# Optimization experiments

Measured on AMD Instinct MI355X. Metric: run time of the kernel, lower is better.

Reference implementation:

```python
import jax, jax.numpy as jnp
import numpy as np
from itertools import combinations

Nt, Nrf, Nk, FEAT, BATCH = 64, 4, 8, 512, 1024
Ng = Nt // Nk                      # 8
_MAX = len(list(combinations(range(Ng), Nrf)))  # 70
CSETSIZE = int(2 ** np.floor(np.log2(_MAX)))    # 64
SQRT_NRF = np.float32(np.sqrt(Nrf))


def _generate_antenna_selection_set(num_target):
    """Max-hamming-distance antenna selection set (numpy, matches torch code)."""
    combs = list(combinations(range(Ng), Nrf))
    maxSize = len(combs)
    globalSet = np.zeros((maxSize, Nt, Nrf), np.float32)
    for i, act in enumerate(combs):
        for j, a in enumerate(act):
            globalSet[i, a * Nk:a * Nk + Nk, j] = 1.0
    gsum = globalSet.sum(-1)  # (maxSize, Nt)
    selectSet = np.zeros((num_target, Nt, Nrf), np.float32)
    available = []
    for idx in range(num_target):
        if len(available) == 0:
            available = list(range(maxSize))
        if idx == 0:
            hd = np.zeros(len(available))
        else:
            sel = selectSet[:idx].sum(-1)            # (idx, Nt)
            cand = gsum[np.array(available)]          # (nAvail, Nt)
            hd = (sel[None, :, :] != cand[:, None, :]).sum(axis=(1, 2))
        sid = available[int(np.argmax(hd))]
        selectSet[idx] = globalSet[sid]
        available.remove(sid)
    return selectSet


def setup_inputs() -> dict:
    key = jax.random.key(0)
    ks = jax.random.split(key, 7)
    s = 1.0 / np.sqrt(FEAT)
    DDIM = CSETSIZE * Nrf * Nrf
    return {
        "x": jax.random.normal(ks[0], (BATCH, FEAT), jnp.float32),
        "W_A": jax.random.normal(ks[1], (Nt, FEAT), jnp.float32) * s,
        "b_A": jax.random.normal(ks[2], (Nt,), jnp.float32) * s,
        "W_Dr": jax.random.normal(ks[3], (DDIM, FEAT), jnp.float32) * s,
        "b_Dr": jax.random.normal(ks[4], (DDIM,), jnp.float32) * s,
        "W_Di": jax.random.normal(ks[5], (DDIM, FEAT), jnp.float32) * s,
        "b_Di": jax.random.normal(ks[6], (DDIM,), jnp.float32) * s,
        "CSet": jnp.asarray(_generate_antenna_selection_set(CSETSIZE)),
    }


def reference(x, W_A, b_A, W_Dr, b_Dr, W_Di, b_Di, CSet):
    B = x.shape[0]
    theta = x @ W_A.T + b_A                          # (B, Nt)
    cosT, sinT = jnp.cos(theta), jnp.sin(theta)
    eye = jnp.eye(Nt, dtype=x.dtype)
    A_real = (cosT[:, :, None] * eye)[:, None]       # (B, 1, Nt, Nt) diag-embed
    A_imag = (sinT[:, :, None] * eye)[:, None]
    D_real = (x @ W_Dr.T + b_Dr).reshape(B, CSETSIZE, Nrf, Nrf)
    D_imag = (x @ W_Di.T + b_Di).reshape(B, CSETSIZE, Nrf, Nrf)
    # diag(cos) @ C == row-scale of C (identical math to the dense matmul)
    ArC = cosT[:, None, :, None] * CSet[None]        # (B, CSetSize, Nt, Nrf)
    AiC = sinT[:, None, :, None] * CSet[None]
    ArCDr = ArC @ D_real
    ArCDi = ArC @ D_imag
    AiCDr = AiC @ D_real
    AiCDi = AiC @ D_imag
    V_real = ArCDr - AiCDi                           # (B, CSetSize, Nt, Nrf)
    V_imag = ArCDi + AiCDr
    V_F = jnp.sqrt(jnp.sum(V_real ** 2 + V_imag ** 2, axis=(2, 3)))
    V_F = V_F[:, :, None, None]
    D_real_n = SQRT_NRF * D_real / V_F
    D_imag_n = SQRT_NRF * D_imag / V_F
    return (A_real, A_imag, D_real_n, D_imag_n, CSet)
```

## Files before the change

### kernel.cpp

```cpp
#include <hip/hip_runtime.h>
#include <math.h>

#define BATCH 1024
#define FEAT  512
#define NT    64
#define DDIM  1024

typedef __attribute__((ext_vector_type(8))) short  short8;
typedef __attribute__((ext_vector_type(4))) short  short4v;
typedef __attribute__((ext_vector_type(4))) float  floatx4;

#define AIMG_OFF  0
#define BIMG_OFF  1048576
#define THETA_OFF 3276800

__device__ __forceinline__ unsigned short bf16rne(float f) {
    unsigned int u = __float_as_uint(f);
    return (unsigned short)((u + 0x7fffu + ((u >> 16) & 1u)) >> 16);
}
__device__ __forceinline__ short4v pack4(const float4 a) {
    short4v r;
    r[0] = (short)bf16rne(a.x); r[1] = (short)bf16rne(a.y);
    r[2] = (short)bf16rne(a.z); r[3] = (short)bf16rne(a.w);
    return r;
}

__device__ __forceinline__ void gld16(const unsigned char* g, unsigned char* l) {
    __builtin_amdgcn_global_load_lds(
        (const __attribute__((address_space(1))) unsigned int*)g,
        (__attribute__((address_space(3))) unsigned int*)l, 16, 0, 0);
}


__global__ __launch_bounds__(256) void k0_prep(
    const float* __restrict__ x,
    const float* __restrict__ W_A,  const float* __restrict__ b_A,
    const float* __restrict__ W_Dr, const float* __restrict__ W_Di,
    const float* __restrict__ cset,
    unsigned char* __restrict__ ws, float* __restrict__ out)
{
    __shared__ __align__(16) unsigned short As[64][40];
    __shared__ __align__(16) unsigned short Bs[64][40];

    const int bid = blockIdx.x;
    const int tid = threadIdx.x;

    if (bid < 256) {
        unsigned short* aimg = (unsigned short*)(ws + AIMG_OFF);
        unsigned short* bimg = (unsigned short*)(ws + BIMG_OFF);
        const int gtid = bid * 256 + tid;
        for (int idx = gtid; idx < 196608; idx += 65536) {
            const float* src;
            unsigned short* dst;
            if (idx < 65536) {
                const int rt = idx >> 12, kb = (idx >> 9) & 7;
                const int r  = (idx >> 3) & 63, c = idx & 7;
                src = x + ((size_t)(rt * 64 + r) * FEAT + kb * 64 + c * 8);
                dst = aimg + ((rt * 8 + kb) * 4096 + r * 64 + ((c ^ (r & 7)) * 8));
            } else {
                const int j  = idx - 65536;
                const int ct = j >> 12, kb = (j >> 9) & 7;
                const int n  = (j >> 3) & 63, c = j & 7;
                const int g = n >> 5, h = (n >> 4) & 1, pos = n & 15;
                const float* wrow =
                    (h ? W_Di : W_Dr) + (size_t)(ct * 32 + g * 16 + pos) * FEAT;
                src = wrow + kb * 64 + c * 8;
                dst = bimg + ((ct * 8 + kb) * 4096 + n * 64 + ((c ^ (n & 7)) * 8));
            }
            const float4 v0 = *(const float4*)src;
            const float4 v1 = *(const float4*)(src + 4);
            short8 o;
            o[0] = (short)bf16rne(v0.x); o[1] = (short)bf16rne(v0.y);
            o[2] = (short)bf16rne(v0.z); o[3] = (short)bf16rne(v0.w);
            o[4] = (short)bf16rne(v1.x); o[5] = (short)bf16rne(v1.y);
            o[6] = (short)bf16rne(v1.z); o[7] = (short)bf16rne(v1.w);
            *(short8*)dst = o;
        }
    } else if (bid < 272) {
        float* theta_ws = (float*)(ws + THETA_OFF);
        const int lane = tid & 63;
        const int wv   = tid >> 6;
        const int ln   = lane & 15;
        const int quad = lane >> 4;
        const int f = tid & 7;
        const int r = tid >> 3;
        const int row0 = (bid - 256) * 64;

        const float* arow0 = x + (size_t)(row0 + r) * FEAT;
        const float* arow1 = x + (size_t)(row0 + r + 32) * FEAT;
        const float* brow0 = W_A + (size_t)r * FEAT;
        const float* brow1 = W_A + (size_t)(r + 32) * FEAT;

        float4 pa0 = *(const float4*)(arow0 + f * 4);
        float4 pa1 = *(const float4*)(arow1 + f * 4);
        float4 pb0 = *(const float4*)(brow0 + f * 4);
        float4 pb1 = *(const float4*)(brow1 + f * 4);

        floatx4 acc[4] = {{0,0,0,0},{0,0,0,0},{0,0,0,0},{0,0,0,0}};

        #pragma unroll 1
        for (int it = 0; it < 16; ++it) {
            __syncthreads();
            *(short4v*)&As[r][f * 4]      = pack4(pa0);
            *(short4v*)&As[r + 32][f * 4] = pack4(pa1);
            *(short4v*)&Bs[r][f * 4]      = pack4(pb0);
            *(short4v*)&Bs[r + 32][f * 4] = pack4(pb1);
            __syncthreads();
            if (it < 15) {
                const int ko = (it + 1) * 32 + f * 4;
                pa0 = *(const float4*)(arow0 + ko);
                pa1 = *(const float4*)(arow1 + ko);
                pb0 = *(const float4*)(brow0 + ko);
                pb1 = *(const float4*)(brow1 + ko);
            }
            const short8 a = *(const short8*)&As[wv * 16 + ln][quad * 8];
            #pragma unroll
            for (int t = 0; t < 4; ++t) {
                const short8 b = *(const short8*)&Bs[t * 16 + ln][quad * 8];
                acc[t] = __builtin_amdgcn_mfma_f32_16x16x32_bf16(a, b, acc[t], 0, 0, 0);
            }
        }
        #pragma unroll
        for (int t = 0; t < 4; ++t) {
            const int colg = t * 16 + ln;
            const float ba = b_A[colg];
            #pragma unroll
            for (int i = 0; i < 4; ++i) {
                const int row_g = row0 + wv * 16 + quad * 4 + i;
                theta_ws[row_g * NT + colg] = acc[t][i] + ba;
            }
        }
    } else {
        const int cb = bid - 272;
        const size_t base = (size_t)2 * BATCH * 4096 + (size_t)2 * BATCH * DDIM;
        ((float4*)(out + base))[cb * 256 + tid] = ((const float4*)cset)[cb * 256 + tid];
    }
}

__global__ __launch_bounds__(256) void k1_main(
    const unsigned char* __restrict__ ws,
    const float* __restrict__ b_Dr, const float* __restrict__ b_Di,
    float* __restrict__ out)
{
    __shared__ __align__(16) unsigned char smem[32768];

    const int bid = blockIdx.x;
    const int tid = threadIdx.x;

    if (bid < 512) {
        const int rt   = bid & 15;
        const int ct   = bid >> 4;
        const int lane = tid & 63;
        const int wv   = tid >> 6;
        const int ln   = lane & 15;
        const int quad = lane >> 4;
        const int row0 = rt * 64;

        const unsigned char* Atiles = ws + AIMG_OFF + (size_t)rt * 8 * 8192;
        const unsigned char* Btiles = ws + BIMG_OFF + (size_t)ct * 8 * 8192;

        const int g0 = (wv * 2 + 0) * 1024;
        const int g1 = (wv * 2 + 1) * 1024;
        const int lo = lane * 16;

        floatx4 acc[4] = {{0,0,0,0},{0,0,0,0},{0,0,0,0},{0,0,0,0}};

        {
            unsigned char* La = smem;
            unsigned char* Lb = smem + 8192;
            gld16(Atiles + g0 + lo, La + g0);
            gld16(Atiles + g1 + lo, La + g1);
            gld16(Btiles + g0 + lo, Lb + g0);
            gld16(Btiles + g1 + lo, Lb + g1);
        }

        const int rowOffA = (wv * 16 + ln) * 128;
        const int swz = ln & 7;
        int cur = 0;

        #pragma unroll 1
        for (int kb = 0; kb < 8; ++kb) {
            __syncthreads();
            if (kb < 7) {
                const unsigned char* At = Atiles + (kb + 1) * 8192;
                const unsigned char* Bt = Btiles + (kb + 1) * 8192;
                unsigned char* La = smem + (cur ^ 1) * 16384;
                unsigned char* Lb = La + 8192;
                gld16(At + g0 + lo, La + g0);
                gld16(At + g1 + lo, La + g1);
                gld16(Bt + g0 + lo, Lb + g0);
                gld16(Bt + g1 + lo, Lb + g1);
            }
            const unsigned char* La = smem + cur * 16384;
            const unsigned char* Lb = La + 8192;
            #pragma unroll
            for (int ks = 0; ks < 2; ++ks) {
                const int ca = ((ks * 4 + quad) ^ swz) * 16;
                const short8 a = *(const short8*)(La + rowOffA + ca);
                #pragma unroll
                for (int t = 0; t < 4; ++t) {
                    const short8 b = *(const short8*)(Lb + (t * 16 + ln) * 128 + ca);
                    acc[t] = __builtin_amdgcn_mfma_f32_16x16x32_bf16(a, b, acc[t], 0, 0, 0);
                }
            }
            cur ^= 1;
        }

        const size_t drn = (size_t)2 * BATCH * 4096;
        const size_t din = drn + (size_t)BATCH * DDIM;
        const int woff = ct * 32;
        #pragma unroll
        for (int p = 0; p < 2; ++p) {
            const int colg = woff + p * 16 + ln;
            const float br = b_Dr[colg];
            const float bi = b_Di[colg];
            float dr[4], di[4], ps[4];
            #pragma unroll
            for (int i = 0; i < 4; ++i) {
                dr[i] = acc[2 * p][i] + br;
                di[i] = acc[2 * p + 1][i] + bi;
                ps[i] = dr[i] * dr[i] + di[i] * di[i];
            }
            #pragma unroll
            for (int i = 0; i < 4; ++i) {
                ps[i] += __shfl_xor(ps[i], 1);
                ps[i] += __shfl_xor(ps[i], 2);
                ps[i] += __shfl_xor(ps[i], 4);
                ps[i] += __shfl_xor(ps[i], 8);
            }
            #pragma unroll
            for (int i = 0; i < 4; ++i) {
                const float scale = 2.0f / sqrtf(8.0f * ps[i]);
                const size_t row_g = (size_t)(row0 + wv * 16 + quad * 4 + i);
                out[drn + row_g * DDIM + colg] = dr[i] * scale;
                out[din + row_g * DDIM + colg] = di[i] * scale;
            }
        }
    } else {
        const float* theta_ws = (const float*)(ws + THETA_OFF);
        float* cosT = (float*)smem;
        float* sinT = cosT + NT;
        const int b = bid - 512;

        if (tid < NT) {
            float s, c;
            sincosf(theta_ws[b * NT + tid], &s, &c);
            cosT[tid] = c; sinT[tid] = s;
        }
        __syncthreads();

        float* ar = out + (size_t)b * 4096;
        float* ai = out + (size_t)BATCH * 4096 + (size_t)b * 4096;
        #pragma unroll
        for (int it = 0; it < 4; ++it) {
            const int idx = tid + it * 256;
            const int tt = idx >> 4;
            const int j0 = (idx & 15) * 4;
            float4 vr = {0.f, 0.f, 0.f, 0.f};
            float4 vi = {0.f, 0.f, 0.f, 0.f};
            if (tt >= j0 && tt < j0 + 4) {
                ((float*)&vr)[tt - j0] = cosT[tt];
                ((float*)&vi)[tt - j0] = sinT[tt];
            }
            ((float4*)ar)[idx] = vr;
            ((float4*)ai)[idx] = vi;
        }
    }
}

extern "C" void kernel_launch(void* const* d_in, const int* in_sizes, int n_in,
                              void* d_out, int out_size, void* d_ws, size_t ws_size,
                              hipStream_t stream) {
    const float* x    = (const float*)d_in[0];
    const float* W_A  = (const float*)d_in[1];
    const float* b_A  = (const float*)d_in[2];
    const float* W_Dr = (const float*)d_in[3];
    const float* b_Dr = (const float*)d_in[4];
    const float* W_Di = (const float*)d_in[5];
    const float* b_Di = (const float*)d_in[6];
    const float* CSet = (const float*)d_in[7];
    float* out = (float*)d_out;
    unsigned char* ws = (unsigned char*)d_ws;

    k0_prep<<<288, 256, 0, stream>>>(x, W_A, b_A, W_Dr, W_Di, CSet, ws, out);
    k1_main<<<1536, 256, 0, stream>>>(ws, b_Dr, b_Di, out);
}
```

Measured before the change: 109.6 us.

## Compute theta per batch row inside k1 diag blocks, drop k0 MFMA stage

Removes the bf16 MFMA theta GEMM from the prep kernel and the theta workspace round-trip. Each diagonal-writer block in the main kernel now computes its own 64 theta values with fp32 dot products (4 lanes per output, shuffle reduce) before sincos. This shortens the prep kernel and raises theta precision to fp32. In exchange, every one of the 1024 batch blocks re-reads all of W_A (128 KB) from cache and does more scalar FMA work before writing.

```diff
diff --git a/kernel.cpp b/kernel.cpp
--- a/kernel.cpp
+++ b/kernel.cpp
@@ -7,22 +7,14 @@
 #define DDIM  1024
 
 typedef __attribute__((ext_vector_type(8))) short  short8;
-typedef __attribute__((ext_vector_type(4))) short  short4v;
 typedef __attribute__((ext_vector_type(4))) float  floatx4;
 
 #define AIMG_OFF  0
 #define BIMG_OFF  1048576
-#define THETA_OFF 3276800
 
 __device__ __forceinline__ unsigned short bf16rne(float f) {
     unsigned int u = __float_as_uint(f);
     return (unsigned short)((u + 0x7fffu + ((u >> 16) & 1u)) >> 16);
-}
-__device__ __forceinline__ short4v pack4(const float4 a) {
-    short4v r;
-    r[0] = (short)bf16rne(a.x); r[1] = (short)bf16rne(a.y);
-    r[2] = (short)bf16rne(a.z); r[3] = (short)bf16rne(a.w);
-    return r;
 }
 
 __device__ __forceinline__ void gld16(const unsigned char* g, unsigned char* l) {
@@ -34,14 +26,10 @@
 
 __global__ __launch_bounds__(256) void k0_prep(
     const float* __restrict__ x,
-    const float* __restrict__ W_A,  const float* __restrict__ b_A,
     const float* __restrict__ W_Dr, const float* __restrict__ W_Di,
     const float* __restrict__ cset,
     unsigned char* __restrict__ ws, float* __restrict__ out)
 {
-    __shared__ __align__(16) unsigned short As[64][40];
-    __shared__ __align__(16) unsigned short Bs[64][40];
-
     const int bid = blockIdx.x;
     const int tid = threadIdx.x;
 
@@ -76,62 +64,8 @@
             o[6] = (short)bf16rne(v1.z); o[7] = (short)bf16rne(v1.w);
             *(short8*)dst = o;
         }
-    } else if (bid < 272) {
-        float* theta_ws = (float*)(ws + THETA_OFF);
-        const int lane = tid & 63;
-        const int wv   = tid >> 6;
-        const int ln   = lane & 15;
-        const int quad = lane >> 4;
-        const int f = tid & 7;
-        const int r = tid >> 3;
-        const int row0 = (bid - 256) * 64;
-
-        const float* arow0 = x + (size_t)(row0 + r) * FEAT;
-        const float* arow1 = x + (size_t)(row0 + r + 32) * FEAT;
-        const float* brow0 = W_A + (size_t)r * FEAT;
-        const float* brow1 = W_A + (size_t)(r + 32) * FEAT;
-
-        float4 pa0 = *(const float4*)(arow0 + f * 4);
-        float4 pa1 = *(const float4*)(arow1 + f * 4);
-        float4 pb0 = *(const float4*)(brow0 + f * 4);
-        float4 pb1 = *(const float4*)(brow1 + f * 4);
-
-        floatx4 acc[4] = {{0,0,0,0},{0,0,0,0},{0,0,0,0},{0,0,0,0}};
-
-        #pragma unroll 1
-        for (int it = 0; it < 16; ++it) {
-            __syncthreads();
-            *(short4v*)&As[r][f * 4]      = pack4(pa0);
-            *(short4v*)&As[r + 32][f * 4] = pack4(pa1);
-            *(short4v*)&Bs[r][f * 4]      = pack4(pb0);
-            *(short4v*)&Bs[r + 32][f * 4] = pack4(pb1);
-            __syncthreads();
-            if (it < 15) {
-                const int ko = (it + 1) * 32 + f * 4;
-                pa0 = *(const float4*)(arow0 + ko);
-                pa1 = *(const float4*)(arow1 + ko);
-                pb0 = *(const float4*)(brow0 + ko);
-                pb1 = *(const float4*)(brow1 + ko);
-            }
-            const short8 a = *(const short8*)&As[wv * 16 + ln][quad * 8];
-            #pragma unroll
-            for (int t = 0; t < 4; ++t) {
-                const short8 b = *(const short8*)&Bs[t * 16 + ln][quad * 8];
-                acc[t] = __builtin_amdgcn_mfma_f32_16x16x32_bf16(a, b, acc[t], 0, 0, 0);
-            }
-        }
-        #pragma unroll
-        for (int t = 0; t < 4; ++t) {
-            const int colg = t * 16 + ln;
-            const float ba = b_A[colg];
-            #pragma unroll
-            for (int i = 0; i < 4; ++i) {
-                const int row_g = row0 + wv * 16 + quad * 4 + i;
-                theta_ws[row_g * NT + colg] = acc[t][i] + ba;
-            }
-        }
     } else {
-        const int cb = bid - 272;
+        const int cb = bid - 256;
         const size_t base = (size_t)2 * BATCH * 4096 + (size_t)2 * BATCH * DDIM;
         ((float4*)(out + base))[cb * 256 + tid] = ((const float4*)cset)[cb * 256 + tid];
     }
@@ -139,6 +73,8 @@
 
 __global__ __launch_bounds__(256) void k1_main(
     const unsigned char* __restrict__ ws,
+    const float* __restrict__ x,   const float* __restrict__ W_A,
+    const float* __restrict__ b_A,
     const float* __restrict__ b_Dr, const float* __restrict__ b_Di,
     float* __restrict__ out)
 {
@@ -237,15 +173,35 @@
             }
         }
     } else {
-        const float* theta_ws = (const float*)(ws + THETA_OFF);
         float* cosT = (float*)smem;
         float* sinT = cosT + NT;
         const int b = bid - 512;
-
-        if (tid < NT) {
+        const int t = tid >> 2;
+        const int q = tid & 3;
+
+        const float* wrow = W_A + (size_t)t * FEAT + q * 4;
+        const float* xrow = x   + (size_t)b * FEAT + q * 4;
+        float sum = 0.f;
+        #pragma unroll 1
+        for (int ch = 0; ch < 4; ++ch) {
+            float4 wv4[8], xv4[8];
+            #pragma unroll
+            for (int i = 0; i < 8; ++i) {
+                const int ko = (ch * 8 + i) * 16;
+                wv4[i] = *(const float4*)(wrow + ko);
+                xv4[i] = *(const float4*)(xrow + ko);
+            }
+            #pragma unroll
+            for (int i = 0; i < 8; ++i)
+                sum += wv4[i].x * xv4[i].x + wv4[i].y * xv4[i].y
+                     + wv4[i].z * xv4[i].z + wv4[i].w * xv4[i].w;
+        }
+        sum += __shfl_xor(sum, 1);
+        sum += __shfl_xor(sum, 2);
+        if (q == 0) {
             float s, c;
-            sincosf(theta_ws[b * NT + tid], &s, &c);
-            cosT[tid] = c; sinT[tid] = s;
+            sincosf(sum + b_A[t], &s, &c);
+            cosT[t] = c; sinT[t] = s;
         }
         __syncthreads();
 
@@ -282,6 +238,6 @@
     float* out = (float*)d_out;
     unsigned char* ws = (unsigned char*)d_ws;
 
-    k0_prep<<<288, 256, 0, stream>>>(x, W_A, b_A, W_Dr, W_Di, CSet, ws, out);
-    k1_main<<<1536, 256, 0, stream>>>(ws, b_Dr, b_Di, out);
-}
+    k0_prep<<<272, 256, 0, stream>>>(x, W_Dr, W_Di, CSet, ws, out);
+    k1_main<<<1536, 256, 0, stream>>>(ws, x, W_A, b_A, b_Dr, b_Di, out);
+}
```

Result: no change. 110.9 us (+1.1%).

## Zero diagonal-embed outputs via memset and write only diagonal elements

Applied to the files above, without the earlier changes.

The dense zero-fill of the A_real/A_imag diagonal-embedded matrices moves out of the k1 kernel into a hipMemsetAsync issued before the kernels. k1 now handles 32 batches per block with 8 threads per batch, computes sincos directly, and stores only the 64 diagonal entries per matrix. The grid shrinks from 1536 to 544 blocks. This adds a separate memset over 32MB plus scattered strided stores. Whether the memset fill beats kernel float4 stores is unclear, and the memset runs serialized ahead of k0.

```diff
diff --git a/kernel.cpp b/kernel.cpp
--- a/kernel.cpp
+++ b/kernel.cpp
@@ -238,32 +238,23 @@
         }
     } else {
         const float* theta_ws = (const float*)(ws + THETA_OFF);
-        float* cosT = (float*)smem;
-        float* sinT = cosT + NT;
-        const int b = bid - 512;
-
-        if (tid < NT) {
-            float s, c;
-            sincosf(theta_ws[b * NT + tid], &s, &c);
-            cosT[tid] = c; sinT[tid] = s;
-        }
-        __syncthreads();
+        const int pb   = bid - 512;
+        const int b    = pb * 32 + (tid >> 3);
+        const int tgrp = tid & 7;
+
+        const float4 t0 = *(const float4*)(theta_ws + b * NT + tgrp * 8);
+        const float4 t1 = *(const float4*)(theta_ws + b * NT + tgrp * 8 + 4);
+        const float th[8] = {t0.x, t0.y, t0.z, t0.w, t1.x, t1.y, t1.z, t1.w};
 
         float* ar = out + (size_t)b * 4096;
         float* ai = out + (size_t)BATCH * 4096 + (size_t)b * 4096;
         #pragma unroll
-        for (int it = 0; it < 4; ++it) {
-            const int idx = tid + it * 256;
-            const int tt = idx >> 4;
-            const int j0 = (idx & 15) * 4;
-            float4 vr = {0.f, 0.f, 0.f, 0.f};
-            float4 vi = {0.f, 0.f, 0.f, 0.f};
-            if (tt >= j0 && tt < j0 + 4) {
-                ((float*)&vr)[tt - j0] = cosT[tt];
-                ((float*)&vi)[tt - j0] = sinT[tt];
-            }
-            ((float4*)ar)[idx] = vr;
-            ((float4*)ai)[idx] = vi;
+        for (int i = 0; i < 8; ++i) {
+            const int t = tgrp * 8 + i;
+            float s, c;
+            sincosf(th[i], &s, &c);
+            ar[t * 65] = c;
+            ai[t * 65] = s;
         }
     }
 }
@@ -282,6 +273,8 @@
     float* out = (float*)d_out;
     unsigned char* ws = (unsigned char*)d_ws;
 
+    hipMemsetAsync(out, 0, (size_t)2 * BATCH * 4096 * sizeof(float), stream);
+
     k0_prep<<<288, 256, 0, stream>>>(x, W_A, b_A, W_Dr, W_Di, CSet, ws, out);
-    k1_main<<<1536, 256, 0, stream>>>(ws, b_Dr, b_Di, out);
-}
+    k1_main<<<544, 256, 0, stream>>>(ws, b_Dr, b_Di, out);
+}
```

Result: no change. 107.6 us (-1.8%).
